# Performance work log

Measured on AMD Instinct MI355X. Metric: run time of the kernel, lower is better.

Reference implementation:

```python
import jax, jax.numpy as jnp
import numpy as np

D_MODEL = 512
N_HEADS = 8
D_Q = 64   # d_queries == d_keys
D_V = 64
LN_EPS = 1e-5


def setup_inputs() -> dict:
    key = jax.random.key(0)
    ks = jax.random.split(key, 10)
    N, S = 4, 2048
    x = jax.random.normal(ks[0], (N, S, D_MODEL), dtype=jnp.float32)
    lengths = jax.random.randint(ks[1], (N,), 1, S + 1)  # true lengths in [1, S]
    s = 0.02
    Wq = jax.random.normal(ks[2], (D_MODEL, N_HEADS * D_Q), dtype=jnp.float32) * s
    bq = jnp.zeros((N_HEADS * D_Q,), dtype=jnp.float32)
    Wkv = jax.random.normal(ks[3], (D_MODEL, N_HEADS * (D_Q + D_V)), dtype=jnp.float32) * s
    bkv = jnp.zeros((N_HEADS * (D_Q + D_V),), dtype=jnp.float32)
    Wo = jax.random.normal(ks[4], (N_HEADS * D_V, D_MODEL), dtype=jnp.float32) * s
    bo = jnp.zeros((D_MODEL,), dtype=jnp.float32)
    gamma = jnp.ones((D_MODEL,), dtype=jnp.float32)
    beta = jnp.zeros((D_MODEL,), dtype=jnp.float32)
    return {"x": x, "key_value_sequence_lengths": lengths, "Wq": Wq, "bq": bq,
            "Wkv": Wkv, "bkv": bkv, "Wo": Wo, "bo": bo, "gamma": gamma, "beta": beta}


def reference(x, key_value_sequence_lengths, Wq, bq, Wkv, bkv, Wo, bo, gamma, beta):
    # Decoder self-attention: query_sequences == key_value_sequences == x.
    N, S, _ = x.shape
    H, dq, dv = N_HEADS, D_Q, D_V

    residual = x
    # Pre-LayerNorm (applied to both queries and keys/values since self-attention)
    mu = jnp.mean(x, axis=-1, keepdims=True)
    var = jnp.var(x, axis=-1, keepdims=True)
    xn = (x - mu) * jax.lax.rsqrt(var + LN_EPS) * gamma + beta

    q = (xn @ Wq + bq).reshape(N, S, H, dq).transpose(0, 2, 1, 3)          # (N,H,S,dq)
    kv = xn @ Wkv + bkv
    k = kv[..., : H * dq].reshape(N, S, H, dq).transpose(0, 2, 1, 3)       # (N,H,S,dq)
    v = kv[..., H * dq :].reshape(N, S, H, dv).transpose(0, 2, 1, 3)       # (N,H,S,dv)

    scores = jnp.einsum("nhqd,nhkd->nhqk", q, k) / jnp.sqrt(jnp.float32(dq))  # (N,H,S,S)

    # Padding mask over keys + causal (not-future) mask
    key_pos = jnp.arange(S)
    pad_ok = key_pos[None, None, None, :] < key_value_sequence_lengths[:, None, None, None]
    causal_ok = (key_pos[None, :] <= jnp.arange(S)[:, None])[None, None, :, :]
    mask = pad_ok & causal_ok
    scores = jnp.where(mask, scores, -jnp.inf)

    attn = jax.nn.softmax(scores, axis=-1)
    out = jnp.einsum("nhqk,nhkd->nqhd", attn, v).reshape(N, S, H * dv)
    out = out @ Wo + bo
    return out + residual
```

## Files before the change

### kernel.cpp

```cpp
#include <hip/hip_runtime.h>
#include <hip/hip_bf16.h>

typedef __attribute__((ext_vector_type(4))) float f32x4;
typedef __attribute__((ext_vector_type(16))) float f32x16;
typedef __attribute__((ext_vector_type(8))) short short8;

#define D_MODEL 512
#define SQ 2048
#define NH 8
#define NBATCH 4
#define MROWS (NBATCH * SQ)

#define CHUNKS_PER_NH 72
#define NSLOTS (32 * CHUNKS_PER_NH)

__device__ __forceinline__ ushort f2b(float x) {
  unsigned int u = __float_as_uint(x);
  return (ushort)((u + 0x7fffu + ((u >> 16) & 1u)) >> 16);
}

__device__ __forceinline__ f32x4 mfma16(short8 a, short8 b, f32x4 c) {
  return __builtin_amdgcn_mfma_f32_16x16x32_bf16(a, b, c, 0, 0, 0);
}
__device__ __forceinline__ f32x16 mfma32(short8 a, short8 b, f32x16 c) {
  return __builtin_amdgcn_mfma_f32_32x32x16_bf16(a, b, c, 0, 0, 0);
}

#define GLOAD_LDS16(g, l)                                                      \
  __builtin_amdgcn_global_load_lds(                                            \
      (const __attribute__((address_space(1))) unsigned int*)(g),              \
      (__attribute__((address_space(3))) unsigned int*)(l), 16, 0, 0)

__global__ __launch_bounds__(256) void transpose_w(const float* __restrict__ W,
                                                   ushort* __restrict__ WT,
                                                   int K, int N) {
  __shared__ ushort tile[32][33];
  int n0 = blockIdx.x * 32, k0 = blockIdx.y * 32;
  int tx = threadIdx.x & 31, ty = threadIdx.x >> 5;
#pragma unroll
  for (int i = 0; i < 4; ++i) {
    int k = ty + i * 8;
    tile[tx][k] = f2b(W[(size_t)(k0 + k) * N + n0 + tx]);
  }
  __syncthreads();
#pragma unroll
  for (int i = 0; i < 4; ++i) {
    int nn = ty + i * 8;
    WT[(size_t)(n0 + nn) * K + k0 + tx] = tile[nn][tx];
  }
}

__global__ __launch_bounds__(256) void ln_kernel(const float* __restrict__ x,
                                                 const float* __restrict__ gamma,
                                                 const float* __restrict__ beta,
                                                 ushort* __restrict__ xn) {
  int wid = threadIdx.x >> 6, lane = threadIdx.x & 63;
  int row = blockIdx.x * 4 + wid;
  const float4* xr = (const float4*)(x + (size_t)row * D_MODEL);
  float4 v0 = xr[lane];
  float4 v1 = xr[lane + 64];
  float s = v0.x + v0.y + v0.z + v0.w + v1.x + v1.y + v1.z + v1.w;
  float q = v0.x * v0.x + v0.y * v0.y + v0.z * v0.z + v0.w * v0.w +
            v1.x * v1.x + v1.y * v1.y + v1.z * v1.z + v1.w * v1.w;
#pragma unroll
  for (int m = 1; m < 64; m <<= 1) {
    s += __shfl_xor(s, m, 64);
    q += __shfl_xor(q, m, 64);
  }
  float mu = s * (1.f / 512.f);
  float var = q * (1.f / 512.f) - mu * mu;
  float rs = rsqrtf(var + 1e-5f);
  const float4* g4 = (const float4*)gamma;
  const float4* b4 = (const float4*)beta;
  ushort* out = xn + (size_t)row * D_MODEL;
#pragma unroll
  for (int i = 0; i < 2; ++i) {
    float4 v = i ? v1 : v0;
    float4 gg = g4[lane + i * 64];
    float4 bb = b4[lane + i * 64];
    ushort4 o;
    o.x = f2b((v.x - mu) * rs * gg.x + bb.x);
    o.y = f2b((v.y - mu) * rs * gg.y + bb.y);
    o.z = f2b((v.z - mu) * rs * gg.z + bb.z);
    o.w = f2b((v.w - mu) * rs * gg.w + bb.w);
    *(ushort4*)(out + (lane + i * 64) * 4) = o;
  }
}

__global__ __launch_bounds__(256) void qkv_gemm(
    const ushort* __restrict__ A, const ushort* __restrict__ BT,
    const float* __restrict__ bq, const float* __restrict__ bkv,
    ushort* __restrict__ qbuf, ushort* __restrict__ kvbuf, float qscale) {
  __shared__ __align__(16) ushort As[128 * 32];
  __shared__ __align__(16) ushort Bs[128 * 32];
  const int tid = threadIdx.x, lane = tid & 63, wid = tid >> 6;
  const int g = lane >> 4, r = lane & 15;
  const int wr = wid >> 1, wc = wid & 1;
  const int bm = blockIdx.y * 128, bn = blockIdx.x * 128;

  f32x4 acc[4][4];
#pragma unroll
  for (int a = 0; a < 4; ++a)
#pragma unroll
    for (int b = 0; b < 4; ++b) acc[a][b] = (f32x4){0.f, 0.f, 0.f, 0.f};

  const int srow = 32 * wid + (lane >> 2);
  const int scol = (lane & 3) * 8;
  const ushort* ga = A + (size_t)(bm + srow) * 512 + scol;
  const ushort* gb = BT + (size_t)(bn + srow) * 512 + scol;
  ushort* la = As + 32 * 32 * wid;
  ushort* lb = Bs + 32 * 32 * wid;

  for (int kb = 0; kb < 512; kb += 32) {
    __syncthreads();
    GLOAD_LDS16(ga + kb, la);
    GLOAD_LDS16(ga + kb + 16 * 512, la + 16 * 32);
    GLOAD_LDS16(gb + kb, lb);
    GLOAD_LDS16(gb + kb + 16 * 512, lb + 16 * 32);
    __syncthreads();
    short8 af[4], bf[4];
#pragma unroll
    for (int i2 = 0; i2 < 4; ++i2) {
      af[i2] = *(const short8*)&As[(wr * 64 + i2 * 16 + r) * 32 + g * 8];
      bf[i2] = *(const short8*)&Bs[(wc * 64 + i2 * 16 + r) * 32 + g * 8];
    }
#pragma unroll
    for (int a = 0; a < 4; ++a)
#pragma unroll
      for (int b = 0; b < 4; ++b) acc[a][b] = mfma16(af[a], bf[b], acc[a][b]);
  }

  const bool isQ = (bn < 512);
  const float* bias = isQ ? bq : bkv;
  ushort* dst = isQ ? qbuf : kvbuf;
  const int cb = isQ ? bn : bn - 512;
  const size_t stride = isQ ? 512 : 1024;
  const float scale = isQ ? qscale : 1.0f;

#pragma unroll
  for (int a = 0; a < 4; ++a) {
#pragma unroll
    for (int reg = 0; reg < 4; ++reg) {
      int row = bm + wr * 64 + a * 16 + g * 4 + reg;
#pragma unroll
      for (int b = 0; b < 4; ++b) {
        int col = cb + wc * 64 + b * 16 + r;
        dst[(size_t)row * stride + col] = f2b((acc[a][b][reg] + bias[col]) * scale);
      }
    }
  }
}

__global__ __launch_bounds__(256) void o_gemm(
    const ushort* __restrict__ A, const ushort* __restrict__ BT,
    const float* __restrict__ bias, const float* __restrict__ resid,
    float* __restrict__ outF) {
  __shared__ __align__(16) ushort As[128 * 32];
  __shared__ __align__(16) ushort Bs[128 * 32];
  const int tid = threadIdx.x, lane = tid & 63, wid = tid >> 6;
  const int g = lane >> 4, r = lane & 15;
  const int wr = wid >> 1, wc = wid & 1;
  const int bm = blockIdx.y * 128, bn = blockIdx.x * 128;

  f32x4 acc[4][4];
#pragma unroll
  for (int a = 0; a < 4; ++a)
#pragma unroll
    for (int b = 0; b < 4; ++b) acc[a][b] = (f32x4){0.f, 0.f, 0.f, 0.f};

  const int srow = 32 * wid + (lane >> 2);
  const int scol = (lane & 3) * 8;
  const ushort* ga = A + (size_t)(bm + srow) * 512 + scol;
  const ushort* gb = BT + (size_t)(bn + srow) * 512 + scol;
  ushort* la = As + 32 * 32 * wid;
  ushort* lb = Bs + 32 * 32 * wid;

  for (int kb = 0; kb < 512; kb += 32) {
    __syncthreads();
    GLOAD_LDS16(ga + kb, la);
    GLOAD_LDS16(ga + kb + 16 * 512, la + 16 * 32);
    GLOAD_LDS16(gb + kb, lb);
    GLOAD_LDS16(gb + kb + 16 * 512, lb + 16 * 32);
    __syncthreads();
    short8 af[4], bf[4];
#pragma unroll
    for (int i2 = 0; i2 < 4; ++i2) {
      af[i2] = *(const short8*)&As[(wr * 64 + i2 * 16 + r) * 32 + g * 8];
      bf[i2] = *(const short8*)&Bs[(wc * 64 + i2 * 16 + r) * 32 + g * 8];
    }
#pragma unroll
    for (int a = 0; a < 4; ++a)
#pragma unroll
      for (int b = 0; b < 4; ++b) acc[a][b] = mfma16(af[a], bf[b], acc[a][b]);
  }

#pragma unroll
  for (int a = 0; a < 4; ++a) {
#pragma unroll
    for (int reg = 0; reg < 4; ++reg) {
      int row = bm + wr * 64 + a * 16 + g * 4 + reg;
#pragma unroll
      for (int b = 0; b < 4; ++b) {
        int col = bn + wc * 64 + b * 16 + r;
        outF[(size_t)row * 512 + col] =
            acc[a][b][reg] + bias[col] + resid[(size_t)row * 512 + col];
      }
    }
  }
}

__global__ __launch_bounds__(256) void attn_kernel(
    const ushort* __restrict__ qbuf, const ushort* __restrict__ kvbuf,
    const int* __restrict__ lengths, ushort* __restrict__ partialO,
    float2* __restrict__ mlbuf) {
  __shared__ __align__(16) ushort smem[9728];

  const int tid = threadIdx.x, lane = tid & 63, wid = tid >> 6;
  const int l31 = lane & 31, h = lane >> 5;

  const int bid = blockIdx.x;
  const int xcd = bid & 7;
  const int j = bid >> 3;
  const int grp = j / 72;
  const int L = j - grp * 72;
  const int nh = (grp << 3) | xcd;
  const int n = nh >> 3, head = nh & 7;
  int qi = 0, c = L;
  while (c >= ((qi + 2) >> 1)) { c -= (qi + 2) >> 1; ++qi; }
  const int T = 4 * qi + 4, nch = (qi + 2) >> 1;
  const int t0 = (c * T) / nch;
  const int t1 = ((c + 1) * T) / nch;
  const int slot = nh * CHUNKS_PER_NH + L;

  const int qb = qi * 128;
  const int len = lengths[n];
  const int q0w = qb + 32 * wid;
  const int q_own = q0w + l31;
  const int nt_w_abs = 4 * qi + wid + 1;
  const int tlen = (len + 31) >> 5;
  int nt = min(t1, tlen) - t0;
  if (nt < 0) nt = 0;

  f32x16 o0, o1;
#pragma unroll
  for (int i = 0; i < 16; ++i) { o0[i] = 0.f; o1[i] = 0.f; }
  float m_ = -1e30f, ls = 0.f;

  const int skey = tid >> 3, sc8 = tid & 7;
  const int kp = lane & 15, dvb = wid * 4 + (lane >> 4);
  const int mu = (l31 >> 2) & 3;

  int voff[4];
#pragma unroll
  for (int jj = 0; jj < 4; ++jj) {
    int dv = 4 * dvb + jj;
    voff[jj] = dv * 20 + (((kp >> 2) ^ ((dv >> 2) & 3)) << 2) + (kp & 3);
  }

  const ushort* kvbase = kvbuf + (size_t)n * SQ * 1024 + head * 64;
  const ushort* kSrc = kvbase + (size_t)(t0 * 32 + skey) * 1024 + sc8 * 8;
  const ushort* vSrc = kvbase + 512 + (size_t)(t0 * 32 + 2 * kp) * 1024 + dvb * 4;
  const int kLdsOff = skey * 72 + sc8 * 8;

  if (nt > 0) {
    short8 qf[4];
    {
      const ushort* qp = qbuf + (size_t)(n * SQ + q_own) * 512 + head * 64 + 8 * h;
#pragma unroll
      for (int kc = 0; kc < 4; ++kc) qf[kc] = *(const short8*)(qp + 16 * kc);
    }

    uint4 kA, kB = {};
    uint2 vaA, vbA, vaB = {}, vbB = {};
    kA = *(const uint4*)kSrc;
    vaA = *(const uint2*)vSrc;
    vbA = *(const uint2*)(vSrc + 1024);
    kSrc += 32 * 1024;
    vSrc += 32 * 1024;
    if (nt > 1) {
      kB = *(const uint4*)kSrc;
      vaB = *(const uint2*)vSrc;
      vbB = *(const uint2*)(vSrc + 1024);
      kSrc += 32 * 1024;
      vSrc += 32 * 1024;
    }
    {
      *(uint4*)(smem + kLdsOff) = kA;
      const ushort* a16 = (const ushort*)&vaA;
      const ushort* b16 = (const ushort*)&vbA;
#pragma unroll
      for (int jj = 0; jj < 4; ++jj)
        ((unsigned*)(smem + 4608))[voff[jj]] =
            (unsigned)a16[jj] | ((unsigned)b16[jj] << 16);
    }
    __syncthreads();

    for (int i = 0; i < nt; ++i) {
      const int t = t0 + i;
      const int cur = i & 1;
      if (i + 2 < nt) {
        if (cur == 0) {
          kA = *(const uint4*)kSrc;
          vaA = *(const uint2*)vSrc;
          vbA = *(const uint2*)(vSrc + 1024);
        } else {
          kB = *(const uint4*)kSrc;
          vaB = *(const uint2*)vSrc;
          vbB = *(const uint2*)(vSrc + 1024);
        }
        kSrc += 32 * 1024;
        vSrc += 32 * 1024;
      }

      if (t < nt_w_abs) {
        const int kb = t * 32;
        const ushort* KtB = smem + cur * 2304;
        const ushort* VtB = smem + 4608 + cur * 2560;

        f32x16 s;
#pragma unroll
        for (int i2 = 0; i2 < 16; ++i2) s[i2] = 0.f;
        {
          const ushort* kr_ = KtB + l31 * 72 + 8 * h;
          short8 k0 = *(const short8*)(kr_);
          short8 k1 = *(const short8*)(kr_ + 16);
          short8 k2 = *(const short8*)(kr_ + 32);
          short8 k3 = *(const short8*)(kr_ + 48);
          s = mfma32(k0, qf[0], s);
          s = mfma32(k1, qf[1], s);
          s = mfma32(k2, qf[2], s);
          s = mfma32(k3, qf[3], s);
        }

        if (kb + 31 > q0w || kb + 31 >= len) {
          int keyb = kb + 4 * h;
#pragma unroll
          for (int reg = 0; reg < 16; ++reg) {
            int key = keyb + (reg & 3) + 8 * (reg >> 2);
            bool ok = (key <= q_own) && (key < len);
            s[reg] = ok ? s[reg] : -1e30f;
          }
        }

        float a0 = fmaxf(fmaxf(s[0], s[1]), s[2]);
        float a1 = fmaxf(fmaxf(s[3], s[4]), s[5]);
        float a2 = fmaxf(fmaxf(s[6], s[7]), s[8]);
        float a3 = fmaxf(fmaxf(s[9], s[10]), s[11]);
        float a4 = fmaxf(fmaxf(s[12], s[13]), s[14]);
        float mx = fmaxf(fmaxf(fmaxf(a0, a1), s[15]),
                         fmaxf(fmaxf(a2, a3), a4));
        {
          auto rr = __builtin_amdgcn_permlane32_swap(__float_as_uint(mx),
                                                     __float_as_uint(mx), false, false);
          mx = fmaxf(__uint_as_float(((const unsigned*)&rr)[0]),
                     __uint_as_float(((const unsigned*)&rr)[1]));
        }

        if (!__all(mx <= m_ + 8.0f)) {
          float mn = fmaxf(m_, mx);
          float sf = __builtin_amdgcn_exp2f(m_ - mn);
          m_ = mn;
          ls *= sf;
#pragma unroll
          for (int i2 = 0; i2 < 16; ++i2) { o0[i2] *= sf; o1[i2] *= sf; }
        }

        float p[16];
#pragma unroll
        for (int reg = 0; reg < 16; ++reg)
          p[reg] = __builtin_amdgcn_exp2f(s[reg] - m_);

        float rsum = ((p[0] + p[1]) + (p[2] + p[3])) + ((p[4] + p[5]) + (p[6] + p[7])) +
                     ((p[8] + p[9]) + (p[10] + p[11])) +
                     ((p[12] + p[13]) + (p[14] + p[15]));
        {
          auto rr = __builtin_amdgcn_permlane32_swap(__float_as_uint(rsum),
                                                     __float_as_uint(rsum), false, false);
          rsum = __uint_as_float(((const unsigned*)&rr)[0]) +
                 __uint_as_float(((const unsigned*)&rr)[1]);
        }
        ls += rsum;

        unsigned pk[8];
#pragma unroll
        for (int jj = 0; jj < 8; ++jj)
          pk[jj] = __builtin_amdgcn_perm(__float_as_uint(p[2 * jj + 1]),
                                         __float_as_uint(p[2 * jj]), 0x07060302u);

#pragma unroll
        for (int kc = 0; kc < 2; ++kc) {
          short8 pf;
          ((unsigned*)&pf)[0] = pk[4 * kc + 0];
          ((unsigned*)&pf)[1] = pk[4 * kc + 1];
          ((unsigned*)&pf)[2] = pk[4 * kc + 2];
          ((unsigned*)&pf)[3] = pk[4 * kc + 3];
          const int u0 = ((2 * kc) ^ mu) << 3;
          const ushort* vb0 = VtB + l31 * 40 + 4 * h;
          const ushort* vb1 = VtB + (32 + l31) * 40 + 4 * h;
          short8 vf0, vf1;
          ((uint2*)&vf0)[0] = *(const uint2*)(vb0 + u0);
          ((uint2*)&vf0)[1] = *(const uint2*)(vb0 + (u0 ^ 8));
          ((uint2*)&vf1)[0] = *(const uint2*)(vb1 + u0);
          ((uint2*)&vf1)[1] = *(const uint2*)(vb1 + (u0 ^ 8));
          o0 = mfma32(vf0, pf, o0);
          o1 = mfma32(vf1, pf, o1);
        }
      }

      if (i + 1 < nt) {
        ushort* KtN = smem + (cur ^ 1) * 2304;
        unsigned* VtN = (unsigned*)(smem + 4608 + (cur ^ 1) * 2560);
        if (cur == 0) {
          *(uint4*)(KtN + kLdsOff) = kB;
          const ushort* a16 = (const ushort*)&vaB;
          const ushort* b16 = (const ushort*)&vbB;
#pragma unroll
          for (int jj = 0; jj < 4; ++jj)
            VtN[voff[jj]] = (unsigned)a16[jj] | ((unsigned)b16[jj] << 16);
        } else {
          *(uint4*)(KtN + kLdsOff) = kA;
          const ushort* a16 = (const ushort*)&vaA;
          const ushort* b16 = (const ushort*)&vbA;
#pragma unroll
          for (int jj = 0; jj < 4; ++jj)
            VtN[voff[jj]] = (unsigned)a16[jj] | ((unsigned)b16[jj] << 16);
        }
      }
      __syncthreads();
    }
  }

  const unsigned long long alive = __ballot(ls > 0.f);
  {
    float inv = (ls > 0.f) ? 1.f / ls : 0.f;
    ushort* OtW = smem + wid * (32 * 68);
#pragma unroll
    for (int b = 0; b < 2; ++b) {
#pragma unroll
      for (int reg = 0; reg < 16; reg += 2) {
        float e0 = (b ? o1[reg] : o0[reg]) * inv;
        float e1 = (b ? o1[reg + 1] : o0[reg + 1]) * inv;
        unsigned pko = __builtin_amdgcn_perm(__float_as_uint(e1),
                                             __float_as_uint(e0), 0x07060302u);
        int dv = 32 * b + (reg & 3) + 8 * (reg >> 2) + 4 * h;
        *(unsigned*)(OtW + l31 * 68 + dv) = pko;
      }
    }
    if (h == 0) mlbuf[slot * 128 + 32 * wid + l31] = make_float2(m_, ls);
  }
  __syncthreads();
  if (alive) {
    int r = lane >> 1, sg = lane & 1;
    if ((alive >> r) & 1ULL) {
      const ushort* rp = smem + wid * (32 * 68) + r * 68 + sg * 32;
      uint2 d0 = *(const uint2*)(rp);
      uint2 d1 = *(const uint2*)(rp + 4);
      uint2 d2 = *(const uint2*)(rp + 8);
      uint2 d3 = *(const uint2*)(rp + 12);
      uint2 d4 = *(const uint2*)(rp + 16);
      uint2 d5 = *(const uint2*)(rp + 20);
      uint2 d6 = *(const uint2*)(rp + 24);
      uint2 d7 = *(const uint2*)(rp + 28);
      ushort* gp = partialO + (size_t)slot * 8192 + (32 * wid + r) * 64 + sg * 32;
      *(uint4*)(gp) = make_uint4(d0.x, d0.y, d1.x, d1.y);
      *(uint4*)(gp + 8) = make_uint4(d2.x, d2.y, d3.x, d3.y);
      *(uint4*)(gp + 16) = make_uint4(d4.x, d4.y, d5.x, d5.y);
      *(uint4*)(gp + 24) = make_uint4(d6.x, d6.y, d7.x, d7.y);
    }
  }
}

__global__ __launch_bounds__(256) void attn_combine(
    const ushort* __restrict__ partialO, const float2* __restrict__ mlbuf,
    ushort* __restrict__ attout) {
  const int bx = blockIdx.x;
  const int nh = bx >> 4, qi = bx & 15;
  const int nch = (qi + 2) >> 1;
  const int off = (qi * (qi + 2) + (qi & 1)) >> 2;
  const int n = nh >> 3, head = nh & 7;
  const int slot0 = nh * CHUNKS_PER_NH + off;

  const int tid = threadIdx.x;
  const int r = tid >> 1, half = tid & 1;

  float mstar = -1e30f;
  for (int c = 0; c < nch; ++c) {
    float2 ml = mlbuf[(slot0 + c) * 128 + r];
    mstar = fmaxf(mstar, ml.x);
  }

  float acc[32];
#pragma unroll
  for (int j = 0; j < 32; ++j) acc[j] = 0.f;
  float Lsum = 0.f;

  for (int c = 0; c < nch; ++c) {
    float2 ml = mlbuf[(slot0 + c) * 128 + r];
    if (ml.y > 0.f) {
      float cf = ml.y * __builtin_amdgcn_exp2f(ml.x - mstar);
      Lsum += cf;
      const uint4* p =
          (const uint4*)(partialO + (size_t)(slot0 + c) * 8192 + r * 64 + half * 32);
#pragma unroll
      for (int u = 0; u < 4; ++u) {
        uint4 d = p[u];
        unsigned w[4] = {d.x, d.y, d.z, d.w};
#pragma unroll
        for (int k = 0; k < 4; ++k) {
          acc[u * 8 + 2 * k] += cf * __uint_as_float(w[k] << 16);
          acc[u * 8 + 2 * k + 1] += cf * __uint_as_float(w[k] & 0xffff0000u);
        }
      }
    }
  }

  const float inv = 1.f / Lsum;
  uint4 outw[4];
#pragma unroll
  for (int u = 0; u < 4; ++u) {
    unsigned ww[4];
#pragma unroll
    for (int k = 0; k < 4; ++k) {
      float e0 = acc[u * 8 + 2 * k] * inv;
      float e1 = acc[u * 8 + 2 * k + 1] * inv;
      ww[k] = ((unsigned)f2b(e0)) | (((unsigned)f2b(e1)) << 16);
    }
    outw[u] = make_uint4(ww[0], ww[1], ww[2], ww[3]);
  }
  ushort* gp = attout + (size_t)(n * SQ + qi * 128 + r) * 512 + head * 64 + half * 32;
#pragma unroll
  for (int u = 0; u < 4; ++u) ((uint4*)gp)[u] = outw[u];
}

extern "C" void kernel_launch(void* const* d_in, const int* in_sizes, int n_in,
                              void* d_out, int out_size, void* d_ws, size_t ws_size,
                              hipStream_t stream) {
  const float* x = (const float*)d_in[0];
  const int* lens = (const int*)d_in[1];
  const float* Wq = (const float*)d_in[2];
  const float* bq = (const float*)d_in[3];
  const float* Wkv = (const float*)d_in[4];
  const float* bkv = (const float*)d_in[5];
  const float* Wo = (const float*)d_in[6];
  const float* bo = (const float*)d_in[7];
  const float* gamma = (const float*)d_in[8];
  const float* beta = (const float*)d_in[9];
  float* out = (float*)d_out;

  size_t off = 0;
  auto alloc = [&](size_t bytes) {
    void* p = (char*)d_ws + off;
    off += (bytes + 255) & ~(size_t)255;
    return p;
  };
  ushort* xn = (ushort*)alloc((size_t)MROWS * 512 * 2);
  ushort* qbuf = (ushort*)alloc((size_t)MROWS * 512 * 2);
  ushort* kvbuf = (ushort*)alloc((size_t)MROWS * 1024 * 2);
  ushort* WT = (ushort*)alloc((size_t)1536 * 512 * 2);
  ushort* WoT = (ushort*)alloc((size_t)512 * 512 * 2);
  ushort* partialO = (ushort*)alloc((size_t)NSLOTS * 8192 * 2);
  float2* mlbuf = (float2*)alloc((size_t)NSLOTS * 128 * 8);
  ushort* attout = xn;

  transpose_w<<<dim3(16, 16), 256, 0, stream>>>(Wq, WT, 512, 512);
  transpose_w<<<dim3(32, 16), 256, 0, stream>>>(Wkv, WT + 512 * 512, 512, 1024);
  transpose_w<<<dim3(16, 16), 256, 0, stream>>>(Wo, WoT, 512, 512);

  ln_kernel<<<MROWS / 4, 256, 0, stream>>>(x, gamma, beta, xn);

  qkv_gemm<<<dim3(12, 64), 256, 0, stream>>>(xn, WT, bq, bkv, qbuf, kvbuf,
                                             0.125f * 1.44269504f);

  attn_kernel<<<dim3(NSLOTS), 256, 0, stream>>>(qbuf, kvbuf, lens, partialO, mlbuf);
  attn_combine<<<dim3(512), 256, 0, stream>>>(partialO, mlbuf, attout);

  o_gemm<<<dim3(4, 64), 256, 0, stream>>>(attout, WoT, bo, x, out);
}
```

Baseline: 123.9 us.

## Fuse weight transposes, write single-chunk attention directly, reverse chunk order, set MFMA priority

Merges the three weight-transpose launches into one kernel. Query tiles that have only one KV chunk now write their normalized output straight into the attention output buffer, so the combine kernel skips those tiles (448 blocks instead of 512). Block-to-chunk order is reversed so the long causal chunks start first, and s_setprio raises wave priority around the MFMA sequences. Together these cut launch overhead and combine traffic and aim to reduce tail imbalance. The cost is more branching and a dependency on the combine indexing matching the skipped tiles.

```diff
diff --git a/kernel.cpp b/kernel.cpp
--- a/kernel.cpp
+++ b/kernel.cpp
@@ -31,11 +31,24 @@
       (const __attribute__((address_space(1))) unsigned int*)(g),              \
       (__attribute__((address_space(3))) unsigned int*)(l), 16, 0, 0)
 
-__global__ __launch_bounds__(256) void transpose_w(const float* __restrict__ W,
-                                                   ushort* __restrict__ WT,
-                                                   int K, int N) {
+__global__ __launch_bounds__(256) void transpose_all(
+    const float* __restrict__ Wq, const float* __restrict__ Wkv,
+    const float* __restrict__ Wo, ushort* __restrict__ WT,
+    ushort* __restrict__ WoT) {
   __shared__ ushort tile[32][33];
-  int n0 = blockIdx.x * 32, k0 = blockIdx.y * 32;
+  int b = blockIdx.x;
+  const float* W;
+  ushort* D;
+  int N;
+  if (b < 256) {
+    W = Wq; D = WT; N = 512;
+  } else if (b < 768) {
+    W = Wkv; D = WT + 512 * 512; N = 1024; b -= 256;
+  } else {
+    W = Wo; D = WoT; N = 512; b -= 768;
+  }
+  const int ntx = N >> 5;
+  int n0 = (b % ntx) * 32, k0 = (b / ntx) * 32;
   int tx = threadIdx.x & 31, ty = threadIdx.x >> 5;
 #pragma unroll
   for (int i = 0; i < 4; ++i) {
@@ -46,7 +59,7 @@
 #pragma unroll
   for (int i = 0; i < 4; ++i) {
     int nn = ty + i * 8;
-    WT[(size_t)(n0 + nn) * K + k0 + tx] = tile[nn][tx];
+    D[(size_t)(n0 + nn) * 512 + k0 + tx] = tile[nn][tx];
   }
 }
 
@@ -212,7 +225,7 @@
 __global__ __launch_bounds__(256) void attn_kernel(
     const ushort* __restrict__ qbuf, const ushort* __restrict__ kvbuf,
     const int* __restrict__ lengths, ushort* __restrict__ partialO,
-    float2* __restrict__ mlbuf) {
+    float2* __restrict__ mlbuf, ushort* __restrict__ attout) {
   __shared__ __align__(16) ushort smem[9728];
 
   const int tid = threadIdx.x, lane = tid & 63, wid = tid >> 6;
@@ -222,7 +235,7 @@
   const int xcd = bid & 7;
   const int j = bid >> 3;
   const int grp = j / 72;
-  const int L = j - grp * 72;
+  const int L = 71 - (j - grp * 72);
   const int nh = (grp << 3) | xcd;
   const int n = nh >> 3, head = nh & 7;
   int qi = 0, c = L;
@@ -326,10 +339,12 @@
           short8 k1 = *(const short8*)(kr_ + 16);
           short8 k2 = *(const short8*)(kr_ + 32);
           short8 k3 = *(const short8*)(kr_ + 48);
+          __builtin_amdgcn_s_setprio(1);
           s = mfma32(k0, qf[0], s);
           s = mfma32(k1, qf[1], s);
           s = mfma32(k2, qf[2], s);
           s = mfma32(k3, qf[3], s);
+          __builtin_amdgcn_s_setprio(0);
         }
 
         if (kb + 31 > q0w || kb + 31 >= len) {
@@ -387,6 +402,7 @@
           pk[jj] = __builtin_amdgcn_perm(__float_as_uint(p[2 * jj + 1]),
                                          __float_as_uint(p[2 * jj]), 0x07060302u);
 
+        __builtin_amdgcn_s_setprio(1);
 #pragma unroll
         for (int kc = 0; kc < 2; ++kc) {
           short8 pf;
@@ -405,6 +421,7 @@
           o0 = mfma32(vf0, pf, o0);
           o1 = mfma32(vf1, pf, o1);
         }
+        __builtin_amdgcn_s_setprio(0);
       }
 
       if (i + 1 < nt) {
@@ -446,9 +463,31 @@
         *(unsigned*)(OtW + l31 * 68 + dv) = pko;
       }
     }
-    if (h == 0) mlbuf[slot * 128 + 32 * wid + l31] = make_float2(m_, ls);
+    if (h == 0 && nch > 1)
+      mlbuf[slot * 128 + 32 * wid + l31] = make_float2(m_, ls);
   }
   __syncthreads();
+
+  if (nch == 1) {
+    int r = lane >> 1, sg = lane & 1;
+    const ushort* rp = smem + wid * (32 * 68) + r * 68 + sg * 32;
+    uint2 d0 = *(const uint2*)(rp);
+    uint2 d1 = *(const uint2*)(rp + 4);
+    uint2 d2 = *(const uint2*)(rp + 8);
+    uint2 d3 = *(const uint2*)(rp + 12);
+    uint2 d4 = *(const uint2*)(rp + 16);
+    uint2 d5 = *(const uint2*)(rp + 20);
+    uint2 d6 = *(const uint2*)(rp + 24);
+    uint2 d7 = *(const uint2*)(rp + 28);
+    ushort* gp = attout + (size_t)(n * SQ + qb + 32 * wid + r) * 512 +
+                 head * 64 + sg * 32;
+    *(uint4*)(gp) = make_uint4(d0.x, d0.y, d1.x, d1.y);
+    *(uint4*)(gp + 8) = make_uint4(d2.x, d2.y, d3.x, d3.y);
+    *(uint4*)(gp + 16) = make_uint4(d4.x, d4.y, d5.x, d5.y);
+    *(uint4*)(gp + 24) = make_uint4(d6.x, d6.y, d7.x, d7.y);
+    return;
+  }
+
   if (alive) {
     int r = lane >> 1, sg = lane & 1;
     if ((alive >> r) & 1ULL) {
@@ -474,7 +513,7 @@
     const ushort* __restrict__ partialO, const float2* __restrict__ mlbuf,
     ushort* __restrict__ attout) {
   const int bx = blockIdx.x;
-  const int nh = bx >> 4, qi = bx & 15;
+  const int nh = bx / 14, qi = 2 + (bx % 14);
   const int nch = (qi + 2) >> 1;
   const int off = (qi * (qi + 2) + (qi & 1)) >> 2;
   const int n = nh >> 3, head = nh & 7;
@@ -562,17 +601,16 @@
   float2* mlbuf = (float2*)alloc((size_t)NSLOTS * 128 * 8);
   ushort* attout = xn;
 
-  transpose_w<<<dim3(16, 16), 256, 0, stream>>>(Wq, WT, 512, 512);
-  transpose_w<<<dim3(32, 16), 256, 0, stream>>>(Wkv, WT + 512 * 512, 512, 1024);
-  transpose_w<<<dim3(16, 16), 256, 0, stream>>>(Wo, WoT, 512, 512);
+  transpose_all<<<dim3(1024), 256, 0, stream>>>(Wq, Wkv, Wo, WT, WoT);
 
   ln_kernel<<<MROWS / 4, 256, 0, stream>>>(x, gamma, beta, xn);
 
   qkv_gemm<<<dim3(12, 64), 256, 0, stream>>>(xn, WT, bq, bkv, qbuf, kvbuf,
                                              0.125f * 1.44269504f);
 
-  attn_kernel<<<dim3(NSLOTS), 256, 0, stream>>>(qbuf, kvbuf, lens, partialO, mlbuf);
-  attn_combine<<<dim3(512), 256, 0, stream>>>(partialO, mlbuf, attout);
+  attn_kernel<<<dim3(NSLOTS), 256, 0, stream>>>(qbuf, kvbuf, lens, partialO,
+                                                mlbuf, attout);
+  attn_combine<<<dim3(448), 256, 0, stream>>>(partialO, mlbuf, attout);
 
   o_gemm<<<dim3(4, 64), 256, 0, stream>>>(attout, WoT, bo, x, out);
 }
```

New measurement: 119.3 us. 3.7% less time.
